# Performance work log

Hardware: AMD Instinct MI355X
Metric: run time of the kernel (lower is better)

## Reference

```python
import jax, jax.numpy as jnp
import numpy as np

N, E, F_IN, EC = 3072, 98304, 128, 3
H1, D1 = 4, 8
EC2 = H1 * EC  # 12 = edge_attr_dim2 = edge_attr_dim3
H2, D2 = 1, 8
C1, C2 = 16, 1  # DIFFPool cluster counts
NEG = 0.2


def _add_self_loops(edge_index, edge_attr, n):
    loops = jnp.arange(n, dtype=edge_index.dtype)
    ei = jnp.concatenate([edge_index, jnp.stack([loops, loops])], axis=1)
    ea = jnp.concatenate([edge_attr, jnp.ones((n, edge_attr.shape[1]), edge_attr.dtype)], axis=0)
    return ei, ea


def _egat(x, edge_index, edge_attr, w, a, heads, out_ch, n):
    # GAT-style per-destination softmax attention, modulated per edge-attr channel.
    h = (x @ w).reshape(n, heads, out_ch)                      # [N,H,D]
    row, col = edge_index[0], edge_index[1]
    alpha = jnp.einsum('ehd,hd->eh', jnp.concatenate([h[row], h[col]], axis=-1), a)
    alpha = jax.nn.leaky_relu(alpha, NEG)
    amax = jax.lax.stop_gradient(jax.ops.segment_max(alpha, row, num_segments=n))
    ex = jnp.exp(alpha - amax[row])
    denom = jax.ops.segment_sum(ex, row, num_segments=n)
    alpha = ex / (denom[row] + 1e-16)                          # [E,H]
    att = alpha[:, :, None] * edge_attr[:, None, :]            # [E,H,C]
    msg = att[:, :, :, None] * h[col][:, :, None, :]           # [E,H,C,D]
    out = jax.ops.segment_sum(msg, row, num_segments=n).reshape(n, -1)  # [N, H*C*D]
    return out, att.reshape(att.shape[0], -1)                  # e_new: [E, H*C]


def _diffpool(x, adj, S):
    s = jax.nn.softmax(S, axis=-1)                             # [Nin, Nout]
    x_new = s.T @ x
    adj_new = jnp.einsum('cim,mj->cij', jnp.einsum('ni,cnm->cim', s, adj), s)
    link = jnp.sqrt(jnp.sum((adj - (s @ s.T)[None]) ** 2)) / adj.size
    ent = -jnp.mean(jnp.sum(s * jnp.log(s + 1e-15), axis=-1))
    return x_new, adj_new, link + ent


def setup_inputs():
    key = jax.random.key(0)
    ks = jax.random.split(key, 20)
    row = jax.random.randint(ks[0], (E,), 0, N, dtype=jnp.int32)
    col = (row + jax.random.randint(ks[1], (E,), 1, N, dtype=jnp.int32)) % N  # no self loops
    g = lambda k, sh: jax.random.normal(k, sh, jnp.float32) * 0.1
    return {
        'x': jax.random.normal(ks[2], (N, F_IN), jnp.float32),
        'edge_index': jnp.stack([row, col]),
        'edge_attr': jax.random.uniform(ks[3], (E, EC), dtype=jnp.float32),
        'adj': jax.random.uniform(ks[4], (EC2, N, N), dtype=jnp.float32),
        'w1': g(ks[5], (F_IN, H1 * D1)), 'a1': g(ks[6], (H1, 2 * D1)),
        'w2': g(ks[7], (H1 * D1 * EC, H2 * D2)), 'a2': g(ks[8], (H2, 2 * D2)),
        's1': g(ks[9], (N, C1)), 's2': g(ks[10], (C1, C2)),
        'fc1_w': g(ks[11], (H2 * D2 * EC2, 128)), 'fc1_b': jnp.zeros((128,), jnp.float32),
        'fc2_w': g(ks[12], (128, 32)), 'fc2_b': jnp.zeros((32,), jnp.float32),
        'fc3_w': g(ks[13], (32, 16)), 'fc3_b': jnp.zeros((16,), jnp.float32),
        'fc4_w': g(ks[14], (16, 2)), 'fc4_b': jnp.zeros((2,), jnp.float32),
    }


def reference(x, edge_index, edge_attr, adj, w1, a1, w2, a2, s1, s2,
              fc1_w, fc1_b, fc2_w, fc2_b, fc3_w, fc3_b, fc4_w, fc4_b):
    ei, ea = _add_self_loops(edge_index, edge_attr, N)
    h, e = _egat(x, ei, ea, w1, a1, H1, D1, N)
    h = jax.nn.elu(h)
    h, e = _egat(h, ei, e, w2, a2, H2, D2, N)
    h = jax.nn.elu(h)
    h, adj1, reg1 = _diffpool(h, adj, s1)
    h, adj2, reg2 = _diffpool(h, adj1, s2)
    h = h.reshape(1, -1)                                       # [1, 8*EC2]
    h = jax.nn.elu(h @ fc1_w + fc1_b)
    h = jax.nn.elu(h @ fc2_w + fc2_b)
    h = jax.nn.elu(h @ fc3_w + fc3_b)
    h = h @ fc4_w + fc4_b
    return jax.nn.log_softmax(h, axis=1), reg1, reg2
```

## Files before the change

### kernel.cpp

```cpp
#include <hip/hip_runtime.h>
#include <hip/hip_bf16.h>

#define Nn 3072
#define E_IN 98304
#define EP (E_IN + Nn)
#define CAP 128
#define NNsq ((size_t)Nn * (size_t)Nn)

__device__ __forceinline__ float eluf(float a) { return a > 0.f ? a : (expf(a) - 1.f); }

__global__ __launch_bounds__(256) void k_softmax(const float* __restrict__ s1,
                                                 float* __restrict__ s_soft,
                                                 float* __restrict__ scal) {
    int n = blockIdx.x * 256 + threadIdx.x;
    float v[16], mx = -1e30f;
#pragma unroll
    for (int i = 0; i < 16; i++) { v[i] = s1[n * 16 + i]; mx = fmaxf(mx, v[i]); }
    float s = 0.f;
#pragma unroll
    for (int i = 0; i < 16; i++) { v[i] = expf(v[i] - mx); s += v[i]; }
    float inv = 1.f / s, ent = 0.f;
#pragma unroll
    for (int i = 0; i < 16; i++) {
        float p = v[i] * inv;
        s_soft[n * 16 + i] = p;
        ent += p * logf(p + 1e-15f);
    }
    __shared__ float wsum[4];
    for (int off = 32; off; off >>= 1) ent += __shfl_xor(ent, off);
    if ((threadIdx.x & 63) == 0) wsum[threadIdx.x >> 6] = ent;
    __syncthreads();
    if (threadIdx.x == 0) atomicAdd(&scal[2], wsum[0] + wsum[1] + wsum[2] + wsum[3]);
}

__global__ void k_bucket(const int* __restrict__ ei, int* __restrict__ counts,
                         int* __restrict__ bucket) {
    int e = blockIdx.x * 256 + threadIdx.x;
    if (e >= EP) return;
    int r = (e < E_IN) ? ei[e] : (e - E_IN);
    int pos = atomicAdd(&counts[r], 1);
    if (pos < CAP) bucket[r * CAP + pos] = e;
}

__global__ __launch_bounds__(256) void k_gemm1(const float* __restrict__ x,
                                               const float* __restrict__ w1,
                                               float* __restrict__ h1) {
    __shared__ float xs[8 * 128];
    int n0 = blockIdx.x * 8;
    for (int idx = threadIdx.x; idx < 1024; idx += 256) xs[idx] = x[(size_t)n0 * 128 + idx];
    __syncthreads();
    int r = threadIdx.x >> 5, j = threadIdx.x & 31;
    float acc = 0.f;
#pragma unroll 8
    for (int k = 0; k < 128; k++) acc += xs[r * 128 + k] * w1[k * 32 + j];
    h1[(n0 + r) * 32 + j] = acc;
}

__global__ __launch_bounds__(256) void k_egat1(const int* __restrict__ ei,
                                               const float* __restrict__ ea,
                                               const float* __restrict__ a1,
                                               const float* __restrict__ h1,
                                               const int* __restrict__ counts,
                                               const int* __restrict__ bucket,
                                               float* __restrict__ e1,
                                               float* __restrict__ hL1) {
    __shared__ float a1s[64];
    __shared__ float alphaL[4][CAP][4];
    __shared__ float eaL[4][CAP][3];
    __shared__ int   colL[4][CAP];
    int tid = threadIdx.x, w = tid >> 6, lane = tid & 63;
    if (tid < 64) a1s[tid] = a1[tid];
    __syncthreads();
    int n = blockIdx.x * 4 + w;
    int deg = counts[n]; if (deg > CAP) deg = CAP;
    const int* ei1 = ei + E_IN;
    float src[4];
#pragma unroll
    for (int h = 0; h < 4; h++) {
        float s = 0.f;
#pragma unroll
        for (int d = 0; d < 8; d++) s += h1[n * 32 + h * 8 + d] * a1s[h * 16 + d];
        src[h] = s;
    }
    float exs[4] = {0.f, 0.f, 0.f, 0.f};
    for (int sl = lane; sl < deg; sl += 64) {
        int e = bucket[n * CAP + sl];
        int col = (e < E_IN) ? ei1[e] : n;
        colL[w][sl] = col;
        float hc[32];
#pragma unroll
        for (int d = 0; d < 32; d++) hc[d] = h1[col * 32 + d];
#pragma unroll
        for (int h = 0; h < 4; h++) {
            float t = src[h];
#pragma unroll
            for (int d = 0; d < 8; d++) t += hc[h * 8 + d] * a1s[h * 16 + 8 + d];
            t = t > 0.f ? t : 0.2f * t;
            float ex = expf(t);
            alphaL[w][sl][h] = ex;
            exs[h] += ex;
        }
#pragma unroll
        for (int c = 0; c < 3; c++)
            eaL[w][sl][c] = (e < E_IN) ? ea[(size_t)e * 3 + c] : 1.0f;
    }
#pragma unroll
    for (int h = 0; h < 4; h++) {
        float v = exs[h];
        for (int off = 32; off; off >>= 1) v += __shfl_xor(v, off);
        exs[h] = v + 1e-16f;
    }
    for (int sl = lane; sl < deg; sl += 64) {
        int e = bucket[n * CAP + sl];
        float al[4];
#pragma unroll
        for (int h = 0; h < 4; h++) { al[h] = alphaL[w][sl][h] / exs[h]; alphaL[w][sl][h] = al[h]; }
#pragma unroll
        for (int h = 0; h < 4; h++)
#pragma unroll
            for (int c = 0; c < 3; c++)
                e1[(size_t)e * 12 + h * 3 + c] = al[h] * eaL[w][sl][c];
    }
    __syncthreads();
    for (int o = lane; o < 96; o += 64) {
        int h = o / 24, rem = o % 24, c = rem >> 3, d = rem & 7;
        float acc = 0.f;
        for (int sl = 0; sl < deg; sl++)
            acc += alphaL[w][sl][h] * eaL[w][sl][c] * h1[colL[w][sl] * 32 + h * 8 + d];
        hL1[(size_t)n * 96 + o] = eluf(acc);
    }
}

__global__ __launch_bounds__(256) void k_gemm2(const float* __restrict__ hL1,
                                               const float* __restrict__ w2,
                                               float* __restrict__ h2) {
    int id = blockIdx.x * 256 + threadIdx.x;
    int n = id >> 3, j = id & 7;
    float acc = 0.f;
#pragma unroll 8
    for (int k = 0; k < 96; k++) acc += hL1[(size_t)n * 96 + k] * w2[k * 8 + j];
    h2[n * 8 + j] = acc;
}

__global__ __launch_bounds__(256) void k_egat2(const int* __restrict__ ei,
                                               const float* __restrict__ e1,
                                               const float* __restrict__ a2,
                                               const float* __restrict__ h2,
                                               const int* __restrict__ counts,
                                               const int* __restrict__ bucket,
                                               float* __restrict__ hL2) {
    __shared__ float a2s[16];
    __shared__ float alphaL[4][CAP];
    __shared__ float eL[4][CAP][12];
    __shared__ int   colL[4][CAP];
    int tid = threadIdx.x, w = tid >> 6, lane = tid & 63;
    if (tid < 16) a2s[tid] = a2[tid];
    __syncthreads();
    int n = blockIdx.x * 4 + w;
    int deg = counts[n]; if (deg > CAP) deg = CAP;
    const int* ei1 = ei + E_IN;
    float src = 0.f;
#pragma unroll
    for (int d = 0; d < 8; d++) src += h2[n * 8 + d] * a2s[d];
    float exs = 0.f;
    for (int sl = lane; sl < deg; sl += 64) {
        int e = bucket[n * CAP + sl];
        int col = (e < E_IN) ? ei1[e] : n;
        colL[w][sl] = col;
        float t = src;
#pragma unroll
        for (int d = 0; d < 8; d++) t += h2[col * 8 + d] * a2s[8 + d];
        t = t > 0.f ? t : 0.2f * t;
        float ex = expf(t);
        alphaL[w][sl] = ex; exs += ex;
#pragma unroll
        for (int c = 0; c < 12; c++) eL[w][sl][c] = e1[(size_t)e * 12 + c];
    }
    for (int off = 32; off; off >>= 1) exs += __shfl_xor(exs, off);
    exs += 1e-16f;
    for (int sl = lane; sl < deg; sl += 64) alphaL[w][sl] /= exs;
    __syncthreads();
    for (int o = lane; o < 96; o += 64) {
        int c = o >> 3, d = o & 7;
        float acc = 0.f;
        for (int sl = 0; sl < deg; sl++)
            acc += alphaL[w][sl] * eL[w][sl][c] * h2[colL[w][sl] * 8 + d];
        hL2[(size_t)n * 96 + o] = eluf(acc);
    }
}

__global__ __launch_bounds__(256) void k_adj(const float* __restrict__ adj,
                                             const float* __restrict__ s_soft,
                                             float* __restrict__ tmat,
                                             float* __restrict__ scal) {
    __shared__ float snL[64 * 16];
    __shared__ float wsum[4];
    int tid = threadIdx.x;
    int m = blockIdx.x * 256 + tid;
    int c0 = blockIdx.y * 2, c1 = c0 + 1;
    int n0 = blockIdx.z * 384;
    float sm[16];
#pragma unroll
    for (int i = 0; i < 16; i++) sm[i] = s_soft[m * 16 + i];
    float t0[16], t1[16];
#pragma unroll
    for (int i = 0; i < 16; i++) { t0[i] = 0.f; t1[i] = 0.f; }
    float lsum = 0.f;
    const float* A0 = adj + (size_t)c0 * NNsq;
    const float* A1 = adj + (size_t)c1 * NNsq;
    for (int sub = 0; sub < 6; sub++) {
        int nb = n0 + sub * 64;
        __syncthreads();
        for (int l = tid; l < 1024; l += 256) snL[l] = s_soft[(size_t)nb * 16 + l];
        __syncthreads();
        for (int nn = 0; nn < 64; nn++) {
            size_t rowbase = (size_t)(nb + nn) * Nn + m;
            float a0 = A0[rowbase];
            float a1 = A1[rowbase];
            float P = 0.f;
            const float* sn = &snL[nn * 16];
#pragma unroll
            for (int i = 0; i < 16; i++) P += sn[i] * sm[i];
            float d0 = a0 - P, d1 = a1 - P;
            lsum += d0 * d0 + d1 * d1;
#pragma unroll
            for (int i = 0; i < 16; i++) { t0[i] += sn[i] * a0; t1[i] += sn[i] * a1; }
        }
    }
#pragma unroll
    for (int i = 0; i < 16; i++) {
        atomicAdd(&tmat[((size_t)c0 * 16 + i) * 3072 + m], t0[i]);
        atomicAdd(&tmat[((size_t)c1 * 16 + i) * 3072 + m], t1[i]);
    }
    for (int off = 32; off; off >>= 1) lsum += __shfl_xor(lsum, off);
    if ((tid & 63) == 0) wsum[tid >> 6] = lsum;
    __syncthreads();
    if (tid == 0) atomicAdd(&scal[0], wsum[0] + wsum[1] + wsum[2] + wsum[3]);
}

__global__ __launch_bounds__(256) void k_adj2(const float* __restrict__ tmat,
                                              const float* __restrict__ s_soft,
                                              float* __restrict__ scal) {
    int b = blockIdx.x;
    int tid = threadIdx.x;
    const float* trow = tmat + (size_t)b * 3072;
    float acc[16];
#pragma unroll
    for (int j = 0; j < 16; j++) acc[j] = 0.f;
    for (int m = tid; m < 3072; m += 256) {
        float tv = trow[m];
#pragma unroll
        for (int j = 0; j < 16; j++) acc[j] += tv * s_soft[m * 16 + j];
    }
    __shared__ float wpart[16][4];
#pragma unroll
    for (int j = 0; j < 16; j++) {
        float v = acc[j];
        for (int off = 32; off; off >>= 1) v += __shfl_xor(v, off);
        if ((tid & 63) == 0) wpart[j][tid >> 6] = v;
    }
    __syncthreads();
    if (tid < 16) {
        float v = wpart[tid][0] + wpart[tid][1] + wpart[tid][2] + wpart[tid][3];
        float d = v - 1.0f;
        atomicAdd(&scal[1], d * d);
    }
}

__global__ __launch_bounds__(256) void k_colsum(const float* __restrict__ hL2,
                                                float* __restrict__ xfin) {
    int f = blockIdx.x;
    int tid = threadIdx.x;
    float s = 0.f;
    for (int n = tid; n < 3072; n += 256) s += hL2[(size_t)n * 96 + f];
    __shared__ float wsum[4];
    for (int off = 32; off; off >>= 1) s += __shfl_xor(s, off);
    if ((tid & 63) == 0) wsum[tid >> 6] = s;
    __syncthreads();
    if (tid == 0) xfin[f] = wsum[0] + wsum[1] + wsum[2] + wsum[3];
}

__global__ void k_fc(const float* __restrict__ xfin,
                     const float* __restrict__ w1, const float* __restrict__ b1,
                     const float* __restrict__ w2, const float* __restrict__ b2,
                     const float* __restrict__ w3, const float* __restrict__ b3,
                     const float* __restrict__ w4, const float* __restrict__ b4,
                     const float* __restrict__ scal, float* __restrict__ out) {
    __shared__ float xf[96], z1[128], z2[32], z3[16], z4[2];
    int t = threadIdx.x;
    if (t < 96) xf[t] = xfin[t];
    __syncthreads();
    {
        float a = b1[t];
        for (int k = 0; k < 96; k++) a += xf[k] * w1[k * 128 + t];
        z1[t] = eluf(a);
    }
    __syncthreads();
    if (t < 32) {
        float a = b2[t];
        for (int k = 0; k < 128; k++) a += z1[k] * w2[k * 32 + t];
        z2[t] = eluf(a);
    }
    __syncthreads();
    if (t < 16) {
        float a = b3[t];
        for (int k = 0; k < 32; k++) a += z2[k] * w3[k * 16 + t];
        z3[t] = eluf(a);
    }
    __syncthreads();
    if (t < 2) {
        float a = b4[t];
        for (int k = 0; k < 16; k++) a += z3[k] * w4[k * 2 + t];
        z4[t] = a;
    }
    __syncthreads();
    if (t == 0) {
        float mx = fmaxf(z4[0], z4[1]);
        float lse = mx + logf(expf(z4[0] - mx) + expf(z4[1] - mx));
        out[0] = z4[0] - lse;
        out[1] = z4[1] - lse;
        float ent1 = -scal[2] / 3072.0f;
        float link1 = sqrtf(scal[0]) / 113246208.0f;
        out[2] = link1 + ent1;
        float link2 = sqrtf(scal[1]) / 3072.0f;
        out[3] = link2;
    }
}

extern "C" void kernel_launch(void* const* d_in, const int* in_sizes, int n_in,
                              void* d_out, int out_size, void* d_ws, size_t ws_size,
                              hipStream_t stream) {
    const float* x    = (const float*)d_in[0];
    const int*   ei   = (const int*)d_in[1];
    const float* ea   = (const float*)d_in[2];
    const float* adj  = (const float*)d_in[3];
    const float* w1   = (const float*)d_in[4];
    const float* a1   = (const float*)d_in[5];
    const float* w2   = (const float*)d_in[6];
    const float* a2   = (const float*)d_in[7];
    const float* s1   = (const float*)d_in[8];
    const float* fc1w = (const float*)d_in[10];
    const float* fc1b = (const float*)d_in[11];
    const float* fc2w = (const float*)d_in[12];
    const float* fc2b = (const float*)d_in[13];
    const float* fc3w = (const float*)d_in[14];
    const float* fc3b = (const float*)d_in[15];
    const float* fc4w = (const float*)d_in[16];
    const float* fc4b = (const float*)d_in[17];
    float* out = (float*)d_out;

    float* ws     = (float*)d_ws;
    float* tmat   = ws;
    float* xfin   = tmat + 589824;
    float* scal   = xfin + 96;
    int*   counts = (int*)(scal + 4);
    int*   bucket = counts + 3072;
    float* s_soft = (float*)(bucket + 3072 * CAP);
    float* h1     = s_soft + 3072 * 16;
    float* hL1    = h1 + 3072 * 32;
    float* h2     = hL1 + 3072 * 96;
    float* hL2    = h2 + 3072 * 8;
    float* e1     = hL2 + 3072 * 96;

    hipMemsetAsync(tmat, 0, (589824 + 96 + 4) * sizeof(float) + 3072 * sizeof(int), stream);

    k_softmax<<<12, 256, 0, stream>>>(s1, s_soft, scal);
    k_bucket<<<(EP + 255) / 256, 256, 0, stream>>>(ei, counts, bucket);
    k_gemm1<<<384, 256, 0, stream>>>(x, w1, h1);
    k_egat1<<<768, 256, 0, stream>>>(ei, ea, a1, h1, counts, bucket, e1, hL1);
    k_gemm2<<<96, 256, 0, stream>>>(hL1, w2, h2);
    k_egat2<<<768, 256, 0, stream>>>(ei, e1, a2, h2, counts, bucket, hL2);
    k_adj<<<dim3(12, 6, 8), 256, 0, stream>>>(adj, s_soft, tmat, scal);
    k_adj2<<<192, 256, 0, stream>>>(tmat, s_soft, scal);
    k_colsum<<<96, 256, 0, stream>>>(hL2, xfin);
    k_fc<<<1, 128, 0, stream>>>(xfin, fc1w, fc1b, fc2w, fc2b, fc3w, fc3b, fc4w, fc4b, scal, out);
}
```

Measured before the change: 869.7 us.

## Expand DiffPool link loss algebraically and vectorize adjacency contraction with float4

The per-element link loss ||A - S S^T||^2 is expanded into three terms: sum of A^2, minus twice the trace of S^T A S, plus the channel count times ||S^T S||_F^2. The S^T S term comes from a new small k_psq kernel, and the trace is collected in k_adj2. This removes the 16-FMA per-element P computation from the adjacency streaming kernel. k_adj now handles one channel per block with float4 loads, four columns per thread and a finer n-split. In exchange, far more atomicAdds go to tmat, and the expanded formula may lose some floating-point precision through cancellation.

```diff
diff --git a/kernel.cpp b/kernel.cpp
--- a/kernel.cpp
+++ b/kernel.cpp
@@ -31,6 +31,20 @@
     if ((threadIdx.x & 63) == 0) wsum[threadIdx.x >> 6] = ent;
     __syncthreads();
     if (threadIdx.x == 0) atomicAdd(&scal[2], wsum[0] + wsum[1] + wsum[2] + wsum[3]);
+}
+
+__global__ __launch_bounds__(256) void k_psq(const float* __restrict__ s_soft,
+                                             float* __restrict__ Mbuf) {
+    __shared__ float sL[256 * 16];
+    int tid = threadIdx.x;
+    int n0 = blockIdx.x * 256;
+    for (int l = tid; l < 4096; l += 256) sL[l] = s_soft[(size_t)n0 * 16 + l];
+    __syncthreads();
+    int i = tid >> 4, j = tid & 15;
+    float acc = 0.f;
+#pragma unroll 8
+    for (int n = 0; n < 256; n++) acc += sL[n * 16 + i] * sL[n * 16 + j];
+    atomicAdd(&Mbuf[tid], acc);
 }
 
 __global__ void k_bucket(const int* __restrict__ ei, int* __restrict__ counts,
@@ -189,51 +203,49 @@
     }
 }
 
-__global__ __launch_bounds__(256) void k_adj(const float* __restrict__ adj,
-                                             const float* __restrict__ s_soft,
-                                             float* __restrict__ tmat,
-                                             float* __restrict__ scal) {
-    __shared__ float snL[64 * 16];
+__global__ __launch_bounds__(256, 4) void k_adj(const float* __restrict__ adj,
+                                                const float* __restrict__ s_soft,
+                                                float* __restrict__ tmat,
+                                                float* __restrict__ scal) {
+    __shared__ float snL[96 * 16];
     __shared__ float wsum[4];
     int tid = threadIdx.x;
-    int m = blockIdx.x * 256 + tid;
-    int c0 = blockIdx.y * 2, c1 = c0 + 1;
-    int n0 = blockIdx.z * 384;
-    float sm[16];
-#pragma unroll
-    for (int i = 0; i < 16; i++) sm[i] = s_soft[m * 16 + i];
-    float t0[16], t1[16];
-#pragma unroll
-    for (int i = 0; i < 16; i++) { t0[i] = 0.f; t1[i] = 0.f; }
-    float lsum = 0.f;
-    const float* A0 = adj + (size_t)c0 * NNsq;
-    const float* A1 = adj + (size_t)c1 * NNsq;
-    for (int sub = 0; sub < 6; sub++) {
-        int nb = n0 + sub * 64;
-        __syncthreads();
-        for (int l = tid; l < 1024; l += 256) snL[l] = s_soft[(size_t)nb * 16 + l];
-        __syncthreads();
-        for (int nn = 0; nn < 64; nn++) {
-            size_t rowbase = (size_t)(nb + nn) * Nn + m;
-            float a0 = A0[rowbase];
-            float a1 = A1[rowbase];
-            float P = 0.f;
-            const float* sn = &snL[nn * 16];
-#pragma unroll
-            for (int i = 0; i < 16; i++) P += sn[i] * sm[i];
-            float d0 = a0 - P, d1 = a1 - P;
-            lsum += d0 * d0 + d1 * d1;
-#pragma unroll
-            for (int i = 0; i < 16; i++) { t0[i] += sn[i] * a0; t1[i] += sn[i] * a1; }
+    int m4 = blockIdx.x * 256 + tid;
+    int c  = blockIdx.y;
+    int n0 = blockIdx.z * 96;
+    for (int l = tid; l < 1536; l += 256) snL[l] = s_soft[(size_t)n0 * 16 + l];
+    const float4* A = (const float4*)(adj + (size_t)c * NNsq);
+    float t[16][4];
+#pragma unroll
+    for (int i = 0; i < 16; i++) { t[i][0] = t[i][1] = t[i][2] = t[i][3] = 0.f; }
+    float lsq = 0.f;
+    __syncthreads();
+    size_t base = (size_t)n0 * 768 + m4;
+    for (int nn = 0; nn < 96; nn += 4) {
+        float4 a[4];
+#pragma unroll
+        for (int u = 0; u < 4; u++) a[u] = A[base + (size_t)(nn + u) * 768];
+#pragma unroll
+        for (int u = 0; u < 4; u++) {
+            lsq += a[u].x * a[u].x + a[u].y * a[u].y + a[u].z * a[u].z + a[u].w * a[u].w;
+            const float* sn = &snL[(nn + u) * 16];
+#pragma unroll
+            for (int i = 0; i < 16; i++) {
+                float s = sn[i];
+                t[i][0] += s * a[u].x; t[i][1] += s * a[u].y;
+                t[i][2] += s * a[u].z; t[i][3] += s * a[u].w;
+            }
         }
     }
+    int m = m4 * 4;
 #pragma unroll
     for (int i = 0; i < 16; i++) {
-        atomicAdd(&tmat[((size_t)c0 * 16 + i) * 3072 + m], t0[i]);
-        atomicAdd(&tmat[((size_t)c1 * 16 + i) * 3072 + m], t1[i]);
-    }
-    for (int off = 32; off; off >>= 1) lsum += __shfl_xor(lsum, off);
-    if ((tid & 63) == 0) wsum[tid >> 6] = lsum;
+        float* dst = &tmat[((size_t)c * 16 + i) * 3072 + m];
+        atomicAdd(dst + 0, t[i][0]); atomicAdd(dst + 1, t[i][1]);
+        atomicAdd(dst + 2, t[i][2]); atomicAdd(dst + 3, t[i][3]);
+    }
+    for (int off = 32; off; off >>= 1) lsq += __shfl_xor(lsq, off);
+    if ((tid & 63) == 0) wsum[tid >> 6] = lsq;
     __syncthreads();
     if (tid == 0) atomicAdd(&scal[0], wsum[0] + wsum[1] + wsum[2] + wsum[3]);
 }
@@ -264,6 +276,7 @@
         float v = wpart[tid][0] + wpart[tid][1] + wpart[tid][2] + wpart[tid][3];
         float d = v - 1.0f;
         atomicAdd(&scal[1], d * d);
+        if (tid == (b & 15)) atomicAdd(&scal[3], v);
     }
 }
 
@@ -285,9 +298,17 @@
                      const float* __restrict__ w2, const float* __restrict__ b2,
                      const float* __restrict__ w3, const float* __restrict__ b3,
                      const float* __restrict__ w4, const float* __restrict__ b4,
-                     const float* __restrict__ scal, float* __restrict__ out) {
+                     const float* __restrict__ scal, const float* __restrict__ Mbuf,
+                     float* __restrict__ out) {
     __shared__ float xf[96], z1[128], z2[32], z3[16], z4[2];
+    __shared__ float msqs[2];
     int t = threadIdx.x;
+    {
+        float m1 = Mbuf[t], m2 = Mbuf[t + 128];
+        float msq = m1 * m1 + m2 * m2;
+        for (int off = 32; off; off >>= 1) msq += __shfl_xor(msq, off);
+        if ((t & 63) == 0) msqs[t >> 6] = msq;
+    }
     if (t < 96) xf[t] = xfin[t];
     __syncthreads();
     {
@@ -320,7 +341,9 @@
         out[0] = z4[0] - lse;
         out[1] = z4[1] - lse;
         float ent1 = -scal[2] / 3072.0f;
-        float link1 = sqrtf(scal[0]) / 113246208.0f;
+        float sumP2 = msqs[0] + msqs[1];
+        float linksq = scal[0] - 2.0f * scal[3] + 12.0f * sumP2;
+        float link1 = sqrtf(fmaxf(linksq, 0.f)) / 113246208.0f;
         out[2] = link1 + ent1;
         float link2 = sqrtf(scal[1]) / 3072.0f;
         out[3] = link2;
@@ -353,7 +376,8 @@
     float* tmat   = ws;
     float* xfin   = tmat + 589824;
     float* scal   = xfin + 96;
-    int*   counts = (int*)(scal + 4);
+    float* Mbuf   = scal + 8;
+    int*   counts = (int*)(Mbuf + 256);
     int*   bucket = counts + 3072;
     float* s_soft = (float*)(bucket + 3072 * CAP);
     float* h1     = s_soft + 3072 * 16;
@@ -362,16 +386,17 @@
     float* hL2    = h2 + 3072 * 8;
     float* e1     = hL2 + 3072 * 96;
 
-    hipMemsetAsync(tmat, 0, (589824 + 96 + 4) * sizeof(float) + 3072 * sizeof(int), stream);
+    hipMemsetAsync(tmat, 0, (589824 + 96 + 8 + 256) * sizeof(float) + 3072 * sizeof(int), stream);
 
     k_softmax<<<12, 256, 0, stream>>>(s1, s_soft, scal);
+    k_psq<<<12, 256, 0, stream>>>(s_soft, Mbuf);
     k_bucket<<<(EP + 255) / 256, 256, 0, stream>>>(ei, counts, bucket);
     k_gemm1<<<384, 256, 0, stream>>>(x, w1, h1);
     k_egat1<<<768, 256, 0, stream>>>(ei, ea, a1, h1, counts, bucket, e1, hL1);
     k_gemm2<<<96, 256, 0, stream>>>(hL1, w2, h2);
     k_egat2<<<768, 256, 0, stream>>>(ei, e1, a2, h2, counts, bucket, hL2);
-    k_adj<<<dim3(12, 6, 8), 256, 0, stream>>>(adj, s_soft, tmat, scal);
+    k_adj<<<dim3(3, 12, 32), 256, 0, stream>>>(adj, s_soft, tmat, scal);
     k_adj2<<<192, 256, 0, stream>>>(tmat, s_soft, scal);
     k_colsum<<<96, 256, 0, stream>>>(hL2, xfin);
-    k_fc<<<1, 128, 0, stream>>>(xfin, fc1w, fc1b, fc2w, fc2b, fc3w, fc3b, fc4w, fc4b, scal, out);
-}
+    k_fc<<<1, 128, 0, stream>>>(xfin, fc1w, fc1b, fc2w, fc2b, fc3w, fc3b, fc4w, fc4b, scal, Mbuf, out);
+}
```

After: 945.1 us. 1.09x slower.
